# Kernel tuning notes

Measured on AMD Instinct MI355X. Metric: run time of the kernel, lower is better.

## Reference

```python
import jax, jax.numpy as jnp
import numpy as np

B, S, D = 8, 1024, 1024   # batch, num_spans, span emb dim
P = 4096                  # num span pairs
DR = 512                  # dim_reduce output
DO = 512                  # repr output


def setup_inputs() -> dict:
    key = jax.random.key(0)
    k1, k2, k3, k4 = jax.random.split(key, 4)
    span = jax.random.normal(k1, (B, S, D), dtype=jnp.float32)
    span_pairs = jax.random.randint(k2, (B, P, 2), 0, S, dtype=jnp.int64)
    W1 = jax.random.normal(k3, (D, DR), dtype=jnp.float32) * (1.0 / np.sqrt(D))
    b1 = jnp.zeros((DR,), dtype=jnp.float32)
    Wr = jax.random.normal(k4, (2 * DR, DO), dtype=jnp.float32) * (1.0 / np.sqrt(2 * DR))
    br = jnp.zeros((DO,), dtype=jnp.float32)
    return {"span": span, "span_pairs": span_pairs, "W1": W1, "b1": b1, "Wr": Wr, "br": br}


def reference(span, span_pairs, W1, b1, Wr, br):
    # TimeDistributed dim-reduce FeedForward (shared: separate=False)
    span1 = jax.nn.relu(jnp.einsum('bsd,df->bsf', span, W1) + b1)  # [B,S,DR]
    # batched_index_select of parent/child span embeddings
    idx_p = span_pairs[:, :, 0]  # [B,P]
    idx_c = span_pairs[:, :, 1]
    emb_p = jnp.take_along_axis(span1, idx_p[:, :, None], axis=1)  # [B,P,DR]
    emb_c = jnp.take_along_axis(span1, idx_c[:, :, None], axis=1)
    pair_emb = jnp.concatenate([emb_p, emb_c], axis=-1)            # [B,P,2*DR]
    # TimeDistributed repr FeedForward
    return jax.nn.relu(jnp.einsum('bpd,df->bpf', pair_emb, Wr) + br)  # [B,P,DO]
```

## Files before the change

kernel.cpp:

```cpp
#include <hip/hip_runtime.h>
#include <hip/hip_bf16.h>


#define BM 128
#define BN 128
#define BK 32

typedef __attribute__((ext_vector_type(8))) short s8v;
typedef __attribute__((ext_vector_type(4))) float f4v;

__device__ __forceinline__ unsigned short f2bf(float f) {
    unsigned int u = __float_as_uint(f);
    u += 0x7fffu + ((u >> 16) & 1u);
    return (unsigned short)(u >> 16);
}

__device__ __forceinline__ void gload16(const void* g, void* l) {
    __builtin_amdgcn_global_load_lds(
        (const __attribute__((address_space(1))) void*)g,
        (__attribute__((address_space(3))) void*)l, 16, 0, 0);
}

__global__ void conv_span_k(const float* __restrict__ in, unsigned short* __restrict__ out) {
    size_t i = (size_t)blockIdx.x * blockDim.x + threadIdx.x;
    const f4v* p = (const f4v*)in + i * 2;
    f4v v0 = p[0], v1 = p[1];
    s8v o;
#pragma unroll
    for (int j = 0; j < 4; ++j) {
        o[j]     = (short)f2bf(v0[j]);
        o[4 + j] = (short)f2bf(v1[j]);
    }
    *(s8v*)(out + i * 8) = o;
}

__global__ void transpose_w_k(const float* __restrict__ in, unsigned short* __restrict__ out) {
    __shared__ float tile[32][33];
    int k0 = blockIdx.x * 32, n0 = blockIdx.y * 32;
    int tx = threadIdx.x, ty = threadIdx.y;
    tile[ty][tx] = in[(size_t)(k0 + ty) * 512 + n0 + tx];
    __syncthreads();
    out[(size_t)(n0 + ty) * 1024 + k0 + tx] = f2bf(tile[tx][ty]);
}

template <int MODE>
__global__ __launch_bounds__(256)
void gemm_tile(const unsigned short* __restrict__ Abase,
               const unsigned short* __restrict__ BT,
               const float* __restrict__ bias,
               const int* __restrict__ pairs,
               void* __restrict__ outp) {
    __shared__ unsigned short Asm[BM * BK];
    __shared__ unsigned short Bsm[BN * BK];

    const int t = threadIdx.x;
    const int lane = t & 63;
    const int w = t >> 6;
    const int wr = w >> 1;
    const int wc = w & 1;
    const int bm0 = blockIdx.x * BM;
    const int bn0 = blockIdx.y * BN;

    const int sr = t >> 2;
    const int sk = (t & 3) * 8;

    const unsigned short *aP0, *aP1, *aC0, *aC1;
    if constexpr (MODE == 1) {
        aP0 = Abase + (size_t)(bm0 + sr) * 1024 + sk;
        aP1 = Abase + (size_t)(bm0 + 64 + sr) * 1024 + sk;
        aC0 = aP0; aC1 = aP1;
    } else {
        int g0 = bm0 + sr, g1 = g0 + 64;
        int b0 = g0 >> 12, b1 = g1 >> 12;
        int ip0 = pairs[(size_t)g0 * 2 + 0];
        int ic0 = pairs[(size_t)g0 * 2 + 1];
        int ip1 = pairs[(size_t)g1 * 2 + 0];
        int ic1 = pairs[(size_t)g1 * 2 + 1];
        aP0 = Abase + (size_t)(b0 * 1024 + ip0) * 512 + sk;
        aC0 = Abase + (size_t)(b0 * 1024 + ic0) * 512 + sk;
        aP1 = Abase + (size_t)(b1 * 1024 + ip1) * 512 + sk;
        aC1 = Abase + (size_t)(b1 * 1024 + ic1) * 512 + sk;
    }
    const unsigned short* bP0 = BT + (size_t)(bn0 + sr) * 1024 + sk;
    const unsigned short* bP1 = BT + (size_t)(bn0 + 64 + sr) * 1024 + sk;

    char* aLds0 = (char*)Asm + w * 1024;
    char* aLds1 = (char*)Asm + 4096 + w * 1024;
    char* bLds0 = (char*)Bsm + w * 1024;
    char* bLds1 = (char*)Bsm + 4096 + w * 1024;

    f4v acc[4][4] = {};

    const int kk = (lane >> 4) * 8;
    const int fr = lane & 15;

    for (int k0 = 0; k0 < 1024; k0 += BK) {
        const unsigned short *s0, *s1;
        int ka;
        if constexpr (MODE == 2) {
            if (k0 < 512) { s0 = aP0; s1 = aP1; ka = k0; }
            else          { s0 = aC0; s1 = aC1; ka = k0 - 512; }
        } else {
            s0 = aP0; s1 = aP1; ka = k0;
        }

        __syncthreads();
        gload16(s0 + ka, aLds0);
        gload16(s1 + ka, aLds1);
        gload16(bP0 + k0, bLds0);
        gload16(bP1 + k0, bLds1);
        __syncthreads();

        s8v af[4], bb[4];
#pragma unroll
        for (int m = 0; m < 4; ++m)
            af[m] = *(const s8v*)&Asm[(wr * 64 + m * 16 + fr) * BK + kk];
#pragma unroll
        for (int n = 0; n < 4; ++n)
            bb[n] = *(const s8v*)&Bsm[(wc * 64 + n * 16 + fr) * BK + kk];
#pragma unroll
        for (int m = 0; m < 4; ++m)
#pragma unroll
            for (int n = 0; n < 4; ++n)
                acc[m][n] = __builtin_amdgcn_mfma_f32_16x16x32_bf16(af[m], bb[n], acc[m][n], 0, 0, 0);
    }

    const int orow0 = bm0 + wr * 64 + (lane >> 4) * 4;
    const int ocol0 = bn0 + wc * 64 + fr;
#pragma unroll
    for (int m = 0; m < 4; ++m) {
#pragma unroll
        for (int n = 0; n < 4; ++n) {
            int col = ocol0 + n * 16;
            float bv = bias[col];
#pragma unroll
            for (int r = 0; r < 4; ++r) {
                int row = orow0 + m * 16 + r;
                float v = fmaxf(acc[m][n][r] + bv, 0.0f);
                if constexpr (MODE == 1)
                    ((unsigned short*)outp)[(size_t)row * 512 + col] = f2bf(v);
                else
                    ((float*)outp)[(size_t)row * 512 + col] = v;
            }
        }
    }
}

extern "C" void kernel_launch(void* const* d_in, const int* in_sizes, int n_in,
                              void* d_out, int out_size, void* d_ws, size_t ws_size,
                              hipStream_t stream) {
    const float* span  = (const float*)d_in[0];
    const int*   pairs = (const int*)d_in[1];
    const float* W1    = (const float*)d_in[2];
    const float* b1    = (const float*)d_in[3];
    const float* Wr    = (const float*)d_in[4];
    const float* br    = (const float*)d_in[5];
    float*       out   = (float*)d_out;

    char* ws = (char*)d_ws;
    unsigned short* spanB = (unsigned short*)ws;
    unsigned short* W1T   = (unsigned short*)(ws + 16777216);
    unsigned short* WrT   = (unsigned short*)(ws + 16777216 + 1048576);
    unsigned short* C1    = (unsigned short*)(ws + 16777216 + 2097152);

    conv_span_k<<<4096, 256, 0, stream>>>(span, spanB);
    transpose_w_k<<<dim3(32, 16), dim3(32, 32), 0, stream>>>(W1, W1T);
    transpose_w_k<<<dim3(32, 16), dim3(32, 32), 0, stream>>>(Wr, WrT);

    gemm_tile<1><<<dim3(64, 4),  256, 0, stream>>>(spanB, W1T, b1, nullptr, C1);
    gemm_tile<2><<<dim3(256, 4), 256, 0, stream>>>(C1,    WrT, br, pairs,   out);
}
```

Baseline: 175.4 us.

## Fuse fp32-to-bf16 span conversion into first GEMM and shrink its N tile

Removes the separate span conversion kernel. The first GEMM now reads fp32 span directly, converts it in registers and writes the bf16 tile to LDS, which avoids writing and re-reading a 16MB bf16 copy. The first GEMM also switches to BN=64 with a swapped grid, giving 512 blocks instead of 256 for better CU occupancy. The LDS layout changes to a fragment-major arrangement. The cost is that A loads in GEMM1 become synchronous register loads rather than async LDS loads, and the fp32 span is read 8 times instead of once.

```diff
diff --git a/kernel.cpp b/kernel.cpp
--- a/kernel.cpp
+++ b/kernel.cpp
@@ -2,8 +2,6 @@
 #include <hip/hip_bf16.h>
 
 
-#define BM 128
-#define BN 128
 #define BK 32
 
 typedef __attribute__((ext_vector_type(8))) short s8v;
@@ -21,19 +19,6 @@
         (__attribute__((address_space(3))) void*)l, 16, 0, 0);
 }
 
-__global__ void conv_span_k(const float* __restrict__ in, unsigned short* __restrict__ out) {
-    size_t i = (size_t)blockIdx.x * blockDim.x + threadIdx.x;
-    const f4v* p = (const f4v*)in + i * 2;
-    f4v v0 = p[0], v1 = p[1];
-    s8v o;
-#pragma unroll
-    for (int j = 0; j < 4; ++j) {
-        o[j]     = (short)f2bf(v0[j]);
-        o[4 + j] = (short)f2bf(v1[j]);
-    }
-    *(s8v*)(out + i * 8) = o;
-}
-
 __global__ void transpose_w_k(const float* __restrict__ in, unsigned short* __restrict__ out) {
     __shared__ float tile[32][33];
     int k0 = blockIdx.x * 32, n0 = blockIdx.y * 32;
@@ -45,92 +30,99 @@
 
 template <int MODE>
 __global__ __launch_bounds__(256)
-void gemm_tile(const unsigned short* __restrict__ Abase,
+void gemm_tile(const void* __restrict__ Ap,
                const unsigned short* __restrict__ BT,
                const float* __restrict__ bias,
                const int* __restrict__ pairs,
                void* __restrict__ outp) {
-    __shared__ unsigned short Asm[BM * BK];
+    constexpr int BN = (MODE == 1) ? 64 : 128;
+    constexpr int NF = BN / 32;
+    __shared__ unsigned short Asm[128 * BK];
     __shared__ unsigned short Bsm[BN * BK];
 
     const int t = threadIdx.x;
     const int lane = t & 63;
     const int w = t >> 6;
-    const int wr = w >> 1;
-    const int wc = w & 1;
-    const int bm0 = blockIdx.x * BM;
-    const int bn0 = blockIdx.y * BN;
+    const int wr = w >> 1, wc = w & 1;
+    const int bm0 = (MODE == 1 ? (int)blockIdx.y : (int)blockIdx.x) * 128;
+    const int bn0 = (MODE == 1 ? (int)blockIdx.x : (int)blockIdx.y) * BN;
 
-    const int sr = t >> 2;
-    const int sk = (t & 3) * 8;
+    const int sl = lane & 15;
+    const int sc = lane >> 4;
 
-    const unsigned short *aP0, *aP1, *aC0, *aC1;
+    const float* aF0 = nullptr; const float* aF1 = nullptr;
+    const unsigned short *aP0=nullptr,*aP1=nullptr,*aC0=nullptr,*aC1=nullptr;
     if constexpr (MODE == 1) {
-        aP0 = Abase + (size_t)(bm0 + sr) * 1024 + sk;
-        aP1 = Abase + (size_t)(bm0 + 64 + sr) * 1024 + sk;
-        aC0 = aP0; aC1 = aP1;
+        aF0 = (const float*)Ap + (size_t)(bm0 + w * 16 + sl) * 1024 + sc * 8;
+        aF1 = aF0 + (size_t)64 * 1024;
     } else {
-        int g0 = bm0 + sr, g1 = g0 + 64;
+        int g0 = bm0 + w * 16 + sl, g1 = g0 + 64;
         int b0 = g0 >> 12, b1 = g1 >> 12;
-        int ip0 = pairs[(size_t)g0 * 2 + 0];
-        int ic0 = pairs[(size_t)g0 * 2 + 1];
-        int ip1 = pairs[(size_t)g1 * 2 + 0];
-        int ic1 = pairs[(size_t)g1 * 2 + 1];
-        aP0 = Abase + (size_t)(b0 * 1024 + ip0) * 512 + sk;
-        aC0 = Abase + (size_t)(b0 * 1024 + ic0) * 512 + sk;
-        aP1 = Abase + (size_t)(b1 * 1024 + ip1) * 512 + sk;
-        aC1 = Abase + (size_t)(b1 * 1024 + ic1) * 512 + sk;
+        int ip0 = pairs[g0 * 2 + 0], ic0 = pairs[g0 * 2 + 1];
+        int ip1 = pairs[g1 * 2 + 0], ic1 = pairs[g1 * 2 + 1];
+        const unsigned short* C1b = (const unsigned short*)Ap;
+        aP0 = C1b + (size_t)(b0 * 1024 + ip0) * 512 + sc * 8;
+        aC0 = C1b + (size_t)(b0 * 1024 + ic0) * 512 + sc * 8;
+        aP1 = C1b + (size_t)(b1 * 1024 + ip1) * 512 + sc * 8;
+        aC1 = C1b + (size_t)(b1 * 1024 + ic1) * 512 + sc * 8;
     }
-    const unsigned short* bP0 = BT + (size_t)(bn0 + sr) * 1024 + sk;
-    const unsigned short* bP1 = BT + (size_t)(bn0 + 64 + sr) * 1024 + sk;
+    const unsigned short* bS0 = BT + (size_t)(bn0 + w * 16 + sl) * 1024 + sc * 8;
+    const unsigned short* bS1 = BT + (size_t)(bn0 + 64 + w * 16 + sl) * 1024 + sc * 8;
 
-    char* aLds0 = (char*)Asm + w * 1024;
-    char* aLds1 = (char*)Asm + 4096 + w * 1024;
-    char* bLds0 = (char*)Bsm + w * 1024;
-    char* bLds1 = (char*)Bsm + 4096 + w * 1024;
+    unsigned short* aL0 = Asm + w * 512;
+    unsigned short* aL1 = Asm + (4 + w) * 512;
+    unsigned short* bL0 = Bsm + w * 512;
+    unsigned short* bL1 = Bsm + (4 + w) * 512;
 
-    f4v acc[4][4] = {};
-
-    const int kk = (lane >> 4) * 8;
-    const int fr = lane & 15;
+    f4v acc[4][NF] = {};
 
     for (int k0 = 0; k0 < 1024; k0 += BK) {
-        const unsigned short *s0, *s1;
-        int ka;
-        if constexpr (MODE == 2) {
+        __syncthreads();
+        if constexpr (MODE == 1) {
+            f4v u0 = *(const f4v*)(aF0 + k0);
+            f4v u1 = *(const f4v*)(aF0 + k0 + 4);
+            f4v u2 = *(const f4v*)(aF1 + k0);
+            f4v u3 = *(const f4v*)(aF1 + k0 + 4);
+            gload16(bS0 + k0, bL0);
+            s8v o0, o1;
+#pragma unroll
+            for (int j = 0; j < 4; ++j) {
+                o0[j] = (short)f2bf(u0[j]); o0[4 + j] = (short)f2bf(u1[j]);
+                o1[j] = (short)f2bf(u2[j]); o1[4 + j] = (short)f2bf(u3[j]);
+            }
+            *(s8v*)(aL0 + lane * 8) = o0;
+            *(s8v*)(aL1 + lane * 8) = o1;
+        } else {
+            const unsigned short *s0, *s1; int ka;
             if (k0 < 512) { s0 = aP0; s1 = aP1; ka = k0; }
             else          { s0 = aC0; s1 = aC1; ka = k0 - 512; }
-        } else {
-            s0 = aP0; s1 = aP1; ka = k0;
+            gload16(s0 + ka, aL0);
+            gload16(s1 + ka, aL1);
+            gload16(bS0 + k0, bL0);
+            gload16(bS1 + k0, bL1);
         }
-
-        __syncthreads();
-        gload16(s0 + ka, aLds0);
-        gload16(s1 + ka, aLds1);
-        gload16(bP0 + k0, bLds0);
-        gload16(bP1 + k0, bLds1);
         __syncthreads();
 
-        s8v af[4], bb[4];
+        s8v af[4], bb[NF];
 #pragma unroll
         for (int m = 0; m < 4; ++m)
-            af[m] = *(const s8v*)&Asm[(wr * 64 + m * 16 + fr) * BK + kk];
+            af[m] = *(const s8v*)&Asm[(wr * 4 + m) * 512 + sc * 128 + sl * 8];
 #pragma unroll
-        for (int n = 0; n < 4; ++n)
-            bb[n] = *(const s8v*)&Bsm[(wc * 64 + n * 16 + fr) * BK + kk];
+        for (int n = 0; n < NF; ++n)
+            bb[n] = *(const s8v*)&Bsm[(wc * NF + n) * 512 + sc * 128 + sl * 8];
 #pragma unroll
         for (int m = 0; m < 4; ++m)
 #pragma unroll
-            for (int n = 0; n < 4; ++n)
+            for (int n = 0; n < NF; ++n)
                 acc[m][n] = __builtin_amdgcn_mfma_f32_16x16x32_bf16(af[m], bb[n], acc[m][n], 0, 0, 0);
     }
 
-    const int orow0 = bm0 + wr * 64 + (lane >> 4) * 4;
-    const int ocol0 = bn0 + wc * 64 + fr;
+    const int orow0 = bm0 + wr * 64 + sc * 4;
+    const int ocol0 = bn0 + wc * (BN / 2) + sl;
 #pragma unroll
     for (int m = 0; m < 4; ++m) {
 #pragma unroll
-        for (int n = 0; n < 4; ++n) {
+        for (int n = 0; n < NF; ++n) {
             int col = ocol0 + n * 16;
             float bv = bias[col];
 #pragma unroll
@@ -158,15 +150,13 @@
     float*       out   = (float*)d_out;
 
     char* ws = (char*)d_ws;
-    unsigned short* spanB = (unsigned short*)ws;
-    unsigned short* W1T   = (unsigned short*)(ws + 16777216);
-    unsigned short* WrT   = (unsigned short*)(ws + 16777216 + 1048576);
-    unsigned short* C1    = (unsigned short*)(ws + 16777216 + 2097152);
+    unsigned short* W1T = (unsigned short*)ws;
+    unsigned short* WrT = (unsigned short*)(ws + 1048576);
+    unsigned short* C1  = (unsigned short*)(ws + 2097152);
 
-    conv_span_k<<<4096, 256, 0, stream>>>(span, spanB);
     transpose_w_k<<<dim3(32, 16), dim3(32, 32), 0, stream>>>(W1, W1T);
     transpose_w_k<<<dim3(32, 16), dim3(32, 32), 0, stream>>>(Wr, WrT);
 
-    gemm_tile<1><<<dim3(64, 4),  256, 0, stream>>>(spanB, W1T, b1, nullptr, C1);
-    gemm_tile<2><<<dim3(256, 4), 256, 0, stream>>>(C1,    WrT, br, pairs,   out);
+    gemm_tile<1><<<dim3(8, 64),  256, 0, stream>>>(span, W1T, b1, nullptr, C1);
+    gemm_tile<2><<<dim3(256, 4), 256, 0, stream>>>(C1,   WrT, br, pairs,   out);
 }
```

After: 218.7 us. 1.25x slower.
